# Kernel optimization log

Measured on AMD Instinct MI355X. Metric: run time of the kernel, lower is better.

## Reference

```python
import jax, jax.numpy as jnp
import numpy as np

SEQ_LEN = 8192
HEAD_DIM = 128


def setup_inputs() -> dict:
    key = jax.random.key(0)
    kq, kk, kv = jax.random.split(key, 3)
    q = jax.random.normal(kq, (SEQ_LEN, HEAD_DIM), dtype=jnp.float32)
    k = jax.random.normal(kk, (SEQ_LEN, HEAD_DIM), dtype=jnp.float32)
    v = jax.random.normal(kv, (SEQ_LEN, HEAD_DIM), dtype=jnp.float32)
    return {"q": q, "k": k, "v": v}


def reference(q, k, v):
    # FlashAttention computes exact softmax attention; the blocked loops with
    # online max/sum rescaling in the source are an exact reformulation of:
    #   O = softmax(Q K^T) V
    # NOTE: the original module applies no 1/sqrt(d) scaling, so neither do we.
    s = jnp.einsum('nd,md->nm', q, k)          # [N, N] scores
    p = jax.nn.softmax(s, axis=-1)             # stable softmax (online in src)
    return jnp.einsum('nm,md->nd', p, v)       # [N, d]
```

## Files before the change

kernel.cpp:

```cpp
#include <hip/hip_runtime.h>

#define N_SEQ 8192
#define HDIM  128

typedef _Float16 half8v  __attribute__((ext_vector_type(8)));
typedef float    floatx16 __attribute__((ext_vector_type(16)));
typedef unsigned int uint32;

__global__ void prep_kv(const float* __restrict__ K, const float* __restrict__ V,
                        _Float16* __restrict__ K16s, _Float16* __restrict__ Vs) {
    __shared__ float Kl[32 * 132];
    __shared__ float Vl[32 * 132];
    const int t  = threadIdx.x;
    const int nt = blockIdx.x;
    const int n0 = nt * 32;
    #pragma unroll
    for (int kk = 0; kk < 4; kk++) {
        int idx = t + 256 * kk;
        int nl = idx >> 5, c4 = idx & 31;
        float4 f = *(((const float4*)(K + (size_t)(n0 + nl) * HDIM)) + c4);
        float* dk = &Kl[nl * 132 + c4 * 4];
        dk[0] = f.x; dk[1] = f.y; dk[2] = f.z; dk[3] = f.w;
        float4 g = *(((const float4*)(V + (size_t)(n0 + nl) * HDIM)) + c4);
        float* dv = &Vl[nl * 132 + c4 * 4];
        dv[0] = g.x; dv[1] = g.y; dv[2] = g.z; dv[3] = g.w;
    }
    __syncthreads();
    #pragma unroll
    for (int rep = 0; rep < 2; rep++) {
        int ch = t + rep * 256;
        int kc = ch >> 6, lane = ch & 63, l31 = lane & 31, q5 = (lane >> 5) & 1;
        half8v h;
        #pragma unroll
        for (int j = 0; j < 8; j++) h[j] = (_Float16)Kl[l31 * 132 + kc * 16 + q5 * 8 + j];
        *(half8v*)(K16s + (((size_t)nt * 8 + kc) * 64 + lane) * 8) = h;
    }
    #pragma unroll
    for (int rep = 0; rep < 2; rep++) {
        int ch = t + rep * 256;
        int dt = ch >> 7, kc2 = (ch >> 6) & 1, lane = ch & 63, l31 = lane & 31, q5 = (lane >> 5) & 1;
        half8v h;
        #pragma unroll
        for (int j = 0; j < 8; j++) h[j] = (_Float16)Vl[(kc2 * 16 + q5 * 8 + j) * 132 + dt * 32 + l31];
        *(half8v*)(Vs + ((((size_t)nt * 4 + dt) * 2 + kc2) * 64 + lane) * 8) = h;
    }
}

static __device__ __forceinline__ void stage_tile(
        const _Float16* __restrict__ K16s, const _Float16* __restrict__ Vs,
        _Float16* lds, size_t nt, int wv, int lane) {
    #pragma unroll
    for (int i = 0; i < 4; i++) {
        const int c = wv * 4 + i;
        const _Float16* base = (c < 8) ? (K16s + (nt * 8 + c) * 512)
                                       : (Vs + (nt * 8 + (size_t)(c - 8)) * 512);
        __builtin_amdgcn_global_load_lds(
            (const __attribute__((address_space(1))) void*)(base + lane * 8),
            (__attribute__((address_space(3))) void*)(lds + c * 512),
            16, 0, 0);
    }
}

static __device__ __forceinline__ void do_pv(const half8v (&vsrc)[8], const uint32 (&hpk)[8],
                                             floatx16 (&oacc)[4], int q5) {
    #pragma unroll
    for (int kc2 = 0; kc2 < 2; kc2++) {
        uint32 pass0 = q5 ? hpk[4 * kc2 + 0] : hpk[4 * kc2 + 2];
        uint32 pass1 = q5 ? hpk[4 * kc2 + 1] : hpk[4 * kc2 + 3];
        uint32 r0 = (uint32)__shfl_xor((int)pass0, 32, 64);
        uint32 r1 = (uint32)__shfl_xor((int)pass1, 32, 64);
        uint32 b0 = q5 ? r0 : hpk[4 * kc2 + 0];
        uint32 b1 = q5 ? r1 : hpk[4 * kc2 + 1];
        uint32 b2 = q5 ? hpk[4 * kc2 + 2] : r0;
        uint32 b3 = q5 ? hpk[4 * kc2 + 3] : r1;
        uint4 bu = make_uint4(b0, b1, b2, b3);
        half8v bfrag = __builtin_bit_cast(half8v, bu);
        #pragma unroll
        for (int dt = 0; dt < 4; dt++)
            oacc[dt] = __builtin_amdgcn_mfma_f32_32x32x16_f16(vsrc[dt * 2 + kc2], bfrag, oacc[dt], 0, 0, 0);
    }
}

template <bool DO_PV>
static __device__ __forceinline__ void pipe_step(
        const half8v (&qf)[8], half8v (&vin)[8], const half8v (&vprev)[8],
        floatx16 (&oacc)[4], uint32 (&hpk)[8],
        float& runm, float& lsum, float& palpha, bool& pflag,
        const _Float16* lds, int lane, int q5) {
    half8v kf[8];
    #pragma unroll
    for (int kc = 0; kc < 8; kc++)
        kf[kc] = *(const half8v*)(lds + kc * 512 + lane * 8);
    #pragma unroll
    for (int j = 0; j < 8; j++)
        vin[j] = *(const half8v*)(lds + (8 + j) * 512 + lane * 8);
    if (pflag) {
        #pragma unroll
        for (int dt = 0; dt < 4; dt++)
            #pragma unroll
            for (int r = 0; r < 16; r++) oacc[dt][r] *= palpha;
        pflag = false;
    }
    if (DO_PV) do_pv(vprev, hpk, oacc, q5);
    floatx16 s0, s1;
    #pragma unroll
    for (int r = 0; r < 16; r++) { s0[r] = 0.0f; s1[r] = 0.0f; }
    #pragma unroll
    for (int kc = 0; kc < 4; kc++)
        s0 = __builtin_amdgcn_mfma_f32_32x32x16_f16(kf[kc], qf[kc], s0, 0, 0, 0);
    #pragma unroll
    for (int kc = 4; kc < 8; kc++)
        s1 = __builtin_amdgcn_mfma_f32_32x32x16_f16(kf[kc], qf[kc], s1, 0, 0, 0);
    float sc[16];
    #pragma unroll
    for (int r = 0; r < 16; r++) sc[r] = s0[r] + s1[r];
    float tm[8];
    #pragma unroll
    for (int r = 0; r < 8; r++) tm[r] = fmaxf(sc[r], sc[r + 8]);
    #pragma unroll
    for (int w = 4; w; w >>= 1)
        #pragma unroll
        for (int r = 0; r < w; r++) tm[r] = fmaxf(tm[r], tm[r + w]);
    float cmax = fmaxf(tm[0], __shfl_xor(tm[0], 32, 64));
    if (__any(cmax > runm + 12.0f)) {
        const float mnew = fmaxf(runm, cmax);
        palpha = __builtin_amdgcn_exp2f(runm - mnew);
        runm = mnew;
        lsum *= palpha;
        pflag = true;
    }
    float p[16];
    #pragma unroll
    for (int r = 0; r < 16; r++) p[r] = __builtin_amdgcn_exp2f(sc[r] - runm);
    float ts[8];
    #pragma unroll
    for (int r = 0; r < 8; r++) ts[r] = p[r] + p[r + 8];
    #pragma unroll
    for (int w = 4; w; w >>= 1)
        #pragma unroll
        for (int r = 0; r < w; r++) ts[r] += ts[r + w];
    lsum += ts[0];
    #pragma unroll
    for (int t2 = 0; t2 < 8; t2++) {
        auto pk = __builtin_amdgcn_cvt_pkrtz(p[2 * t2], p[2 * t2 + 1]);
        hpk[t2] = __builtin_bit_cast(uint32, pk);
    }
}

__launch_bounds__(256, 2)
__global__ void fa_main(const float* __restrict__ Qp, const _Float16* __restrict__ K16s,
                        const _Float16* __restrict__ Vs, float* __restrict__ Opart,
                        float* __restrict__ lpart, float* __restrict__ mpart, int tiles) {
    __shared__ _Float16 ldsbuf[2][8192];
    const int tid  = threadIdx.x;
    const int lane = tid & 63;
    const int wv   = tid >> 6;
    const int l31  = lane & 31;
    const int q5   = lane >> 5;
    const int sp   = blockIdx.x;
    const int m0   = blockIdx.y * 128 + wv * 32;
    const float LOG2E = 1.44269504088896f;

    half8v qf[8];
    {
        const float* qrow = Qp + (size_t)(m0 + l31) * HDIM;
        #pragma unroll
        for (int kc = 0; kc < 8; kc++) {
            const float4 a = *(const float4*)(qrow + kc * 16 + q5 * 8);
            const float4 b = *(const float4*)(qrow + kc * 16 + q5 * 8 + 4);
            half8v h;
            h[0] = (_Float16)(a.x * LOG2E); h[1] = (_Float16)(a.y * LOG2E);
            h[2] = (_Float16)(a.z * LOG2E); h[3] = (_Float16)(a.w * LOG2E);
            h[4] = (_Float16)(b.x * LOG2E); h[5] = (_Float16)(b.y * LOG2E);
            h[6] = (_Float16)(b.z * LOG2E); h[7] = (_Float16)(b.w * LOG2E);
            qf[kc] = h;
        }
    }

    floatx16 oacc[4];
    #pragma unroll
    for (int dt = 0; dt < 4; dt++)
        #pragma unroll
        for (int r = 0; r < 16; r++) oacc[dt][r] = 0.0f;

    float runm = -3.0e38f;
    float lsum = 0.0f;
    float palpha = 0.0f;
    bool  pflag = false;
    uint32 hpk[8];
    half8v va[8], vb[8];

    const size_t nt0 = (size_t)sp * tiles;

    stage_tile(K16s, Vs, ldsbuf[0], nt0, wv, lane);
    __syncthreads();
    stage_tile(K16s, Vs, ldsbuf[1], nt0 + 1, wv, lane);
    pipe_step<false>(qf, va, va, oacc, hpk, runm, lsum, palpha, pflag, ldsbuf[0], lane, q5);
    __syncthreads();
    for (int p = 0; p < (tiles - 2) / 2; p++) {
        stage_tile(K16s, Vs, ldsbuf[0], nt0 + 2 + 2 * p, wv, lane);
        pipe_step<true>(qf, vb, va, oacc, hpk, runm, lsum, palpha, pflag, ldsbuf[1], lane, q5);
        __syncthreads();
        stage_tile(K16s, Vs, ldsbuf[1], nt0 + 3 + 2 * p, wv, lane);
        pipe_step<true>(qf, va, vb, oacc, hpk, runm, lsum, palpha, pflag, ldsbuf[0], lane, q5);
        __syncthreads();
    }
    pipe_step<true>(qf, vb, va, oacc, hpk, runm, lsum, palpha, pflag, ldsbuf[1], lane, q5);
    if (pflag) {
        #pragma unroll
        for (int dt = 0; dt < 4; dt++)
            #pragma unroll
            for (int r = 0; r < 16; r++) oacc[dt][r] *= palpha;
    }
    do_pv(vb, hpk, oacc, q5);

    float ltot = lsum + __shfl_xor(lsum, 32, 64);
    if (lane < 32) {
        __builtin_nontemporal_store(ltot, &lpart[(size_t)sp * N_SEQ + m0 + l31]);
        __builtin_nontemporal_store(runm, &mpart[(size_t)sp * N_SEQ + m0 + l31]);
    }
    #pragma unroll
    for (int dt = 0; dt < 4; dt++)
        #pragma unroll
        for (int r = 0; r < 16; r++) {
            int d = dt * 32 + (r & 3) + 8 * (r >> 2) + 4 * q5;
            __builtin_nontemporal_store(oacc[dt][r],
                &Opart[((size_t)sp * HDIM + d) * N_SEQ + m0 + l31]);
        }
}

__global__ void fa_merge(const float* __restrict__ Opart, const float* __restrict__ lpart,
                         const float* __restrict__ mpart, float* __restrict__ Out, int S) {
    __shared__ float lds[64 * 33];
    const int t  = threadIdx.x;
    const int m0 = blockIdx.x * 64;
    const int i  = t & 63;
    const int g  = t >> 6;
    const int m  = m0 + i;
    const int d0 = blockIdx.y * 32 + g * 8;

    float M = -3.0e38f;
    for (int s = 0; s < S; s++) M = fmaxf(M, mpart[(size_t)s * N_SEQ + m]);
    float L = 0.0f;
    for (int s = 0; s < S; s++)
        L += lpart[(size_t)s * N_SEQ + m] * __builtin_amdgcn_exp2f(mpart[(size_t)s * N_SEQ + m] - M);
    const float inv = 1.0f / L;

    float acc[8];
    #pragma unroll
    for (int dd = 0; dd < 8; dd++) acc[dd] = 0.0f;
    for (int s = 0; s < S; s++) {
        const float ww = __builtin_amdgcn_exp2f(mpart[(size_t)s * N_SEQ + m] - M) * inv;
        #pragma unroll
        for (int dd = 0; dd < 8; dd++)
            acc[dd] += __builtin_nontemporal_load(
                &Opart[((size_t)s * HDIM + d0 + dd) * N_SEQ + m]) * ww;
    }
    #pragma unroll
    for (int dd = 0; dd < 8; dd++) lds[i * 33 + g * 8 + dd] = acc[dd];
    __syncthreads();
    const int mi = t >> 2, c = t & 3;
    float4 v0, v1;
    const float* row = &lds[mi * 33 + c * 8];
    v0.x = row[0]; v0.y = row[1]; v0.z = row[2]; v0.w = row[3];
    v1.x = row[4]; v1.y = row[5]; v1.z = row[6]; v1.w = row[7];
    float* outp = Out + (size_t)(m0 + mi) * HDIM + blockIdx.y * 32 + c * 8;
    *(float4*)(outp)     = v0;
    *(float4*)(outp + 4) = v1;
}

__global__ void fa_naive(const float* __restrict__ Q, const float* __restrict__ K,
                         const float* __restrict__ V, float* __restrict__ O) {
    const int m = blockIdx.x;
    const int t = threadIdx.x;
    __shared__ float qs[HDIM];
    __shared__ float ps[256];
    __shared__ float red[256];
    if (t < HDIM) qs[t] = Q[(size_t)m * HDIM + t] * 1.44269504f;
    __syncthreads();
    float om = -3.0e38f, ls = 0.0f, oa = 0.0f;
    for (int nb = 0; nb < N_SEQ; nb += 256) {
        const float* kr = K + (size_t)(nb + t) * HDIM;
        float s = 0.0f;
        #pragma unroll 8
        for (int d = 0; d < HDIM; d++) s += qs[d] * kr[d];
        red[t] = s; __syncthreads();
        for (int st = 128; st > 0; st >>= 1) { if (t < st) red[t] = fmaxf(red[t], red[t + st]); __syncthreads(); }
        float cm = red[0];
        __syncthreads();
        float mn = fmaxf(om, cm);
        float al = __builtin_amdgcn_exp2f(om - mn);
        om = mn;
        float pp = __builtin_amdgcn_exp2f(s - mn);
        ps[t] = pp; red[t] = pp; __syncthreads();
        for (int st = 128; st > 0; st >>= 1) { if (t < st) red[t] += red[t + st]; __syncthreads(); }
        float csum = red[0];
        ls = ls * al + csum;
        if (t < HDIM) {
            float acc = 0.0f;
            for (int j = 0; j < 256; j++) acc += ps[j] * V[(size_t)(nb + j) * HDIM + t];
            oa = oa * al + acc;
        }
        __syncthreads();
    }
    if (t < HDIM) O[(size_t)m * HDIM + t] = oa / ls;
}

extern "C" void kernel_launch(void* const* d_in, const int* in_sizes, int n_in,
                              void* d_out, int out_size, void* d_ws, size_t ws_size,
                              hipStream_t stream) {
    const float* q = (const float*)d_in[0];
    const float* k = (const float*)d_in[1];
    const float* v = (const float*)d_in[2];
    float* out = (float*)d_out;

    const size_t MB = 1024ull * 1024ull;
    int S = 0;
    for (int s = 8; s >= 1; s >>= 1) {
        size_t need = 4 * MB + (size_t)s * (4 * MB + 64 * 1024);
        if (ws_size >= need) { S = s; break; }
    }
    if (S == 0) {
        fa_naive<<<N_SEQ, 256, 0, stream>>>(q, k, v, out);
        return;
    }
    char* ws = (char*)d_ws;
    _Float16* K16s = (_Float16*)ws;
    _Float16* Vs   = (_Float16*)(ws + 2 * MB);
    float* Opart   = (float*)(ws + 4 * MB);
    float* lpart   = (float*)(ws + 4 * MB + (size_t)S * 4 * MB);
    float* mpart   = lpart + (size_t)S * N_SEQ;

    prep_kv<<<dim3(N_SEQ / 32), dim3(256), 0, stream>>>(k, v, K16s, Vs);
    fa_main<<<dim3(S, N_SEQ / 128), dim3(256), 0, stream>>>(q, K16s, Vs, Opart, lpart, mpart, (N_SEQ / 32) / S);
    fa_merge<<<dim3(N_SEQ / 64, HDIM / 32), dim3(256), 0, stream>>>(Opart, lpart, mpart, out, S);
}
```

Measured before the change: 127.7 us.

## Raise fa_main occupancy, allow 16 splits, template merge on split count

After: 456.7 us. +257.6%, slower.

```diff
diff --git a/kernel.cpp b/kernel.cpp
--- a/kernel.cpp
+++ b/kernel.cpp
@@ -147,7 +147,7 @@
     }
 }
 
-__launch_bounds__(256, 2)
+__launch_bounds__(256, 4)
 __global__ void fa_main(const float* __restrict__ Qp, const _Float16* __restrict__ K16s,
                         const _Float16* __restrict__ Vs, float* __restrict__ Opart,
                         float* __restrict__ lpart, float* __restrict__ mpart, int tiles) {
@@ -216,21 +216,21 @@
 
     float ltot = lsum + __shfl_xor(lsum, 32, 64);
     if (lane < 32) {
-        __builtin_nontemporal_store(ltot, &lpart[(size_t)sp * N_SEQ + m0 + l31]);
-        __builtin_nontemporal_store(runm, &mpart[(size_t)sp * N_SEQ + m0 + l31]);
+        lpart[(size_t)sp * N_SEQ + m0 + l31] = ltot;
+        mpart[(size_t)sp * N_SEQ + m0 + l31] = runm;
     }
     #pragma unroll
     for (int dt = 0; dt < 4; dt++)
         #pragma unroll
         for (int r = 0; r < 16; r++) {
             int d = dt * 32 + (r & 3) + 8 * (r >> 2) + 4 * q5;
-            __builtin_nontemporal_store(oacc[dt][r],
-                &Opart[((size_t)sp * HDIM + d) * N_SEQ + m0 + l31]);
+            Opart[((size_t)sp * HDIM + d) * N_SEQ + m0 + l31] = oacc[dt][r];
         }
 }
 
+template <int S>
 __global__ void fa_merge(const float* __restrict__ Opart, const float* __restrict__ lpart,
-                         const float* __restrict__ mpart, float* __restrict__ Out, int S) {
+                         const float* __restrict__ mpart, float* __restrict__ Out) {
     __shared__ float lds[64 * 33];
     const int t  = threadIdx.x;
     const int m0 = blockIdx.x * 64;
@@ -239,22 +239,33 @@
     const int m  = m0 + i;
     const int d0 = blockIdx.y * 32 + g * 8;
 
+    float mv[S], lv[S];
+    #pragma unroll
+    for (int s = 0; s < S; s++) {
+        mv[s] = mpart[(size_t)s * N_SEQ + m];
+        lv[s] = lpart[(size_t)s * N_SEQ + m];
+    }
     float M = -3.0e38f;
-    for (int s = 0; s < S; s++) M = fmaxf(M, mpart[(size_t)s * N_SEQ + m]);
+    #pragma unroll
+    for (int s = 0; s < S; s++) M = fmaxf(M, mv[s]);
+    float wsc[S];
     float L = 0.0f;
-    for (int s = 0; s < S; s++)
-        L += lpart[(size_t)s * N_SEQ + m] * __builtin_amdgcn_exp2f(mpart[(size_t)s * N_SEQ + m] - M);
+    #pragma unroll
+    for (int s = 0; s < S; s++) {
+        wsc[s] = __builtin_amdgcn_exp2f(mv[s] - M);
+        L += lv[s] * wsc[s];
+    }
     const float inv = 1.0f / L;
 
     float acc[8];
     #pragma unroll
     for (int dd = 0; dd < 8; dd++) acc[dd] = 0.0f;
+    #pragma unroll
     for (int s = 0; s < S; s++) {
-        const float ww = __builtin_amdgcn_exp2f(mpart[(size_t)s * N_SEQ + m] - M) * inv;
+        const float ww = wsc[s] * inv;
         #pragma unroll
         for (int dd = 0; dd < 8; dd++)
-            acc[dd] += __builtin_nontemporal_load(
-                &Opart[((size_t)s * HDIM + d0 + dd) * N_SEQ + m]) * ww;
+            acc[dd] += Opart[((size_t)s * HDIM + d0 + dd) * N_SEQ + m] * ww;
     }
     #pragma unroll
     for (int dd = 0; dd < 8; dd++) lds[i * 33 + g * 8 + dd] = acc[dd];
@@ -316,7 +327,7 @@
 
     const size_t MB = 1024ull * 1024ull;
     int S = 0;
-    for (int s = 8; s >= 1; s >>= 1) {
+    for (int s = 16; s >= 1; s >>= 1) {
         size_t need = 4 * MB + (size_t)s * (4 * MB + 64 * 1024);
         if (ws_size >= need) { S = s; break; }
     }
@@ -333,5 +344,12 @@
 
     prep_kv<<<dim3(N_SEQ / 32), dim3(256), 0, stream>>>(k, v, K16s, Vs);
     fa_main<<<dim3(S, N_SEQ / 128), dim3(256), 0, stream>>>(q, K16s, Vs, Opart, lpart, mpart, (N_SEQ / 32) / S);
-    fa_merge<<<dim3(N_SEQ / 64, HDIM / 32), dim3(256), 0, stream>>>(Opart, lpart, mpart, out, S);
-}
+    dim3 mg(N_SEQ / 64, HDIM / 32);
+    switch (S) {
+        case 16: fa_merge<16><<<mg, dim3(256), 0, stream>>>(Opart, lpart, mpart, out); break;
+        case 8:  fa_merge<8> <<<mg, dim3(256), 0, stream>>>(Opart, lpart, mpart, out); break;
+        case 4:  fa_merge<4> <<<mg, dim3(256), 0, stream>>>(Opart, lpart, mpart, out); break;
+        case 2:  fa_merge<2> <<<mg, dim3(256), 0, stream>>>(Opart, lpart, mpart, out); break;
+        default: fa_merge<1> <<<mg, dim3(256), 0, stream>>>(Opart, lpart, mpart, out); break;
+    }
+}
```
